# Kernel optimization log

Hardware: AMD Instinct MI355X
Metric: run time of the kernel (lower is better)

Reference implementation:

```python
import jax, jax.numpy as jnp
import numpy as np

N_NODES = 100000
N_EDGES = 1600000
D_IN = 128
D_HID = 128
D_OUT = 128


def setup_inputs() -> dict:
    key = jax.random.key(0)
    ks = jax.random.split(key, 12)
    x = jax.random.normal(ks[0], (N_NODES, D_IN), dtype=jnp.float32)
    edge_index = jax.random.randint(ks[1], (2, N_EDGES), 0, N_NODES, dtype=jnp.int64)
    s = 0.05
    # GraphConv layer l: out = agg @ w_rel + x @ w_root + b  (lin_rel has bias, lin_root does not)
    w_rel1 = jax.random.normal(ks[2], (D_IN, D_HID), dtype=jnp.float32) * s
    w_root1 = jax.random.normal(ks[3], (D_IN, D_HID), dtype=jnp.float32) * s
    b1 = jax.random.normal(ks[4], (D_HID,), dtype=jnp.float32) * s
    w_rel2 = jax.random.normal(ks[5], (D_HID, D_HID), dtype=jnp.float32) * s
    w_root2 = jax.random.normal(ks[6], (D_HID, D_HID), dtype=jnp.float32) * s
    b2 = jax.random.normal(ks[7], (D_HID,), dtype=jnp.float32) * s
    w_rel3 = jax.random.normal(ks[8], (D_HID, D_OUT), dtype=jnp.float32) * s
    w_root3 = jax.random.normal(ks[9], (D_HID, D_OUT), dtype=jnp.float32) * s
    b3 = jax.random.normal(ks[10], (D_OUT,), dtype=jnp.float32) * s
    return {"x": x, "edge_index": edge_index,
            "w_rel1": w_rel1, "w_root1": w_root1, "b1": b1,
            "w_rel2": w_rel2, "w_root2": w_root2, "b2": b2,
            "w_rel3": w_rel3, "w_root3": w_root3, "b3": b3}


def _graph_conv(h, src, dst, w_rel, w_root, b):
    # sum-aggregate neighbor features (message = x_j, flow src -> dst),
    # then linear; identical math to PyG GraphConv with aggr='add'.
    agg = jax.ops.segment_sum(h[src], dst, num_segments=h.shape[0])
    return agg @ w_rel + h @ w_root + b


def reference(x, edge_index, w_rel1, w_root1, b1, w_rel2, w_root2, b2, w_rel3, w_root3, b3):
    src, dst = edge_index[0], edge_index[1]
    h = jax.nn.relu(_graph_conv(x, src, dst, w_rel1, w_root1, b1))
    h = jax.nn.relu(_graph_conv(h, src, dst, w_rel2, w_root2, b2))
    out = _graph_conv(h, src, dst, w_rel3, w_root3, b3)
    return out
```

## Files before the change

kernel.cpp:

```cpp
#include <hip/hip_runtime.h>
#include <hip/hip_bf16.h>
#include <stdint.h>

typedef __hip_bfloat16 bf16;
typedef __hip_bfloat162 bf162;

typedef __attribute__((ext_vector_type(8))) short short8;
typedef __attribute__((ext_vector_type(4))) float floatx4;

#define BSH   8
#define BSZ   256
#define CHUNK 8192
#define NBMAX 512


__device__ __forceinline__ void acc2(float& a, float& b, unsigned u) {
    a += __uint_as_float(u << 16);
    b += __uint_as_float(u & 0xffff0000u);
}

__global__ __launch_bounds__(256)
void prep_kernel(const float* __restrict__ x, bf16* __restrict__ y, int n4, int nCvt,
                 const float* __restrict__ wr1, const float* __restrict__ wo1,
                 const float* __restrict__ wr2, const float* __restrict__ wo2,
                 const float* __restrict__ wr3, const float* __restrict__ wo3,
                 bf16* __restrict__ w1, bf16* __restrict__ w2, bf16* __restrict__ w3) {
    const int b = blockIdx.x;
    if (b < nCvt) {
        const int i = b * 256 + threadIdx.x;
        if (i < n4) {
            float4 v = ((const float4*)x)[i];
            bf162 a, c;
            a.x = __float2bfloat16(v.x); a.y = __float2bfloat16(v.y);
            c.x = __float2bfloat16(v.z); c.y = __float2bfloat16(v.w);
            ((bf162*)y)[i * 2]     = a;
            ((bf162*)y)[i * 2 + 1] = c;
        }
        return;
    }
    int t = (b - nCvt) * 256 + threadIdx.x;
    const int layer = t >> 12;
    t &= 4095;
    const float* wrel  = (layer == 0) ? wr1 : (layer == 1) ? wr2 : wr3;
    const float* wroot = (layer == 0) ? wo1 : (layer == 1) ? wo2 : wo3;
    bf16*        wsw   = (layer == 0) ? w1  : (layer == 1) ? w2  : w3;
    const int lane = t & 63;
    const int ct   = (t >> 6) & 7;
    const int kt   = t >> 9;
    const int kbase = kt * 32 + (lane >> 4) * 8;
    const int n     = ct * 16 + (lane & 15);
    bf16* q = wsw + (size_t)t * 8;
#pragma unroll
    for (int j = 0; j < 8; ++j) {
        const int k = kbase + j;
        const float v = (k < 128) ? wrel[k * 128 + n] : wroot[(k - 128) * 128 + n];
        q[j] = __float2bfloat16(v);
    }
}


__global__ __launch_bounds__(256)
void bhist_kernel(const int* __restrict__ dst, int* __restrict__ T,
                  int E, int NB, int GB) {
    __shared__ int lh[NBMAX];
    const int b = blockIdx.x;
    for (int u = threadIdx.x; u < NB; u += 256) lh[u] = 0;
    __syncthreads();
    const int beg = b * CHUNK, end = min(beg + CHUNK, E);
    for (int e = beg + threadIdx.x; e < end; e += 256)
        atomicAdd(&lh[dst[e] >> BSH], 1);
    __syncthreads();
    for (int u = threadIdx.x; u < NB; u += 256)
        T[u * GB + b] = lh[u];
}

__global__ __launch_bounds__(256)
void scan1_kernel(const int* __restrict__ deg, int* __restrict__ rp,
                  int* __restrict__ bsum, int n) {
    __shared__ int s[256];
    const int tid = threadIdx.x;
    const int i = blockIdx.x * 256 + tid;
    const int d = (i < n) ? deg[i] : 0;
    s[tid] = d;
    __syncthreads();
    for (int off = 1; off < 256; off <<= 1) {
        int u = (tid >= off) ? s[tid - off] : 0;
        __syncthreads();
        s[tid] += u;
        __syncthreads();
    }
    if (i < n) rp[i] = s[tid] - d;
    if (tid == 255) bsum[blockIdx.x] = s[255];
}

__global__ __launch_bounds__(512)
void scan2_kernel(int* __restrict__ bsum, int G) {
    __shared__ int s[512];
    const int tid = threadIdx.x;
    const int d = (tid < G) ? bsum[tid] : 0;
    s[tid] = d;
    __syncthreads();
    for (int off = 1; off < 512; off <<= 1) {
        int u = (tid >= off) ? s[tid - off] : 0;
        __syncthreads();
        s[tid] += u;
        __syncthreads();
    }
    if (tid < G) bsum[tid] = s[tid] - d;
}

__global__ __launch_bounds__(256)
void scan3_kernel(int* __restrict__ rp, const int* __restrict__ bsum, int n) {
    const int i = blockIdx.x * 256 + threadIdx.x;
    if (i < n) rp[i] += bsum[blockIdx.x];
}

__global__ __launch_bounds__(256)
void bscatter_kernel(const int* __restrict__ src, const int* __restrict__ dst,
                     const int* __restrict__ T, int* __restrict__ ebuf,
                     int E, int NB, int GB) {
    __shared__ int lofs[NBMAX];
    const int b = blockIdx.x;
    for (int u = threadIdx.x; u < NB; u += 256)
        lofs[u] = T[u * GB + b];
    __syncthreads();
    const int beg = b * CHUNK, end = min(beg + CHUNK, E);
    for (int e = beg + threadIdx.x; e < end; e += 256) {
        const int d = dst[e];
        const int u = d >> BSH;
        const int pos = atomicAdd(&lofs[u], 1);
        ebuf[pos] = (src[e] << BSH) | (d & (BSZ - 1));
    }
}

__global__ __launch_bounds__(256)
void bbuild_kernel(const int* __restrict__ T, const int* __restrict__ ebuf,
                   int* __restrict__ rp, int* __restrict__ col,
                   int E, int N, int NB, int GB) {
    __shared__ int s[256];
    __shared__ int lrank[256];
    const int u = blockIdx.x;
    const int tid = threadIdx.x;
    const int beg = T[u * GB];
    const int end = (u + 1 < NB) ? T[(u + 1) * GB] : E;

    lrank[tid] = 0;
    __syncthreads();
    for (int e = beg + tid; e < end; e += 256)
        atomicAdd(&lrank[ebuf[e] & (BSZ - 1)], 1);
    __syncthreads();
    const int cntv = lrank[tid];
    s[tid] = cntv;
    __syncthreads();
    for (int off = 1; off < 256; off <<= 1) {
        int v = (tid >= off) ? s[tid - off] : 0;
        __syncthreads();
        s[tid] += v;
        __syncthreads();
    }
    const int excl = s[tid] - cntv;
    const int node = u * BSZ + tid;
    if (node < N) rp[node] = beg + excl;
    if (u == NB - 1 && tid == 0) rp[N] = E;
    lrank[tid] = beg + excl;
    __syncthreads();
    for (int e = beg + tid; e < end; e += 256) {
        const int p = ebuf[e];
        const int pos = atomicAdd(&lrank[p & (BSZ - 1)], 1);
        col[pos] = p >> BSH;
    }
}


__global__ __launch_bounds__(512)
void agg_kernel(const bf16* __restrict__ h, const int* __restrict__ rp,
                const int* __restrict__ col, bf16* __restrict__ agg, int N) {
    const int lane = threadIdx.x & 63;
    const int wid  = threadIdx.x >> 6;
    const int node = blockIdx.x * 8 + wid;
    if (node >= N) return;
    const int half = lane >> 5;
    const int l32  = lane & 31;
    const int f    = l32 * 4;
    const int beg = rp[node], end = rp[node + 1];

    float acc[4] = {0.f, 0.f, 0.f, 0.f};
    int e = beg;
#pragma unroll 2
    for (; e + 8 <= end; e += 8) {
        const int s0 = col[e + half];
        const int s1 = col[e + 2 + half];
        const int s2 = col[e + 4 + half];
        const int s3 = col[e + 6 + half];
        const uint2 r0 = *(const uint2*)(h + (size_t)s0 * 128 + f);
        const uint2 r1 = *(const uint2*)(h + (size_t)s1 * 128 + f);
        const uint2 r2 = *(const uint2*)(h + (size_t)s2 * 128 + f);
        const uint2 r3 = *(const uint2*)(h + (size_t)s3 * 128 + f);
        acc2(acc[0], acc[1], r0.x); acc2(acc[2], acc[3], r0.y);
        acc2(acc[0], acc[1], r1.x); acc2(acc[2], acc[3], r1.y);
        acc2(acc[0], acc[1], r2.x); acc2(acc[2], acc[3], r2.y);
        acc2(acc[0], acc[1], r3.x); acc2(acc[2], acc[3], r3.y);
    }
    for (; e < end; e += 2) {
        const bool act = (e + half) < end;
        const int s = col[act ? (e + half) : e];
        const uint2 r = *(const uint2*)(h + (size_t)s * 128 + f);
        if (act) { acc2(acc[0], acc[1], r.x); acc2(acc[2], acc[3], r.y); }
    }

#pragma unroll
    for (int j = 0; j < 4; ++j)
        acc[j] += __shfl_xor(acc[j], 32, 64);

    if (half == 0) {
        bf162 o0, o1;
        o0.x = __float2bfloat16(acc[0]); o0.y = __float2bfloat16(acc[1]);
        o1.x = __float2bfloat16(acc[2]); o1.y = __float2bfloat16(acc[3]);
        bf162* q = (bf162*)(agg + (size_t)node * 128 + f);
        q[0] = o0;
        q[1] = o1;
    }
}


template <bool RELU, typename OT>
__global__ __launch_bounds__(256)
void mfma_gemm_kernel(const bf16* __restrict__ Aagg, const bf16* __restrict__ Hroot,
                      const bf16* __restrict__ wsw, const float* __restrict__ bias,
                      OT* __restrict__ out, int M) {
    const int tid  = threadIdx.x;
    const int lane = tid & 63;
    const int wave = tid >> 6;
    const int l15  = lane & 15;
    const int quad = lane >> 4;

    const int row_a = blockIdx.x * 64 + wave * 16 + l15;
    const bool rowok = row_a < M;

    floatx4 acc[8];
#pragma unroll
    for (int ct = 0; ct < 8; ++ct) acc[ct] = (floatx4){0.f, 0.f, 0.f, 0.f};

#pragma unroll
    for (int kt = 0; kt < 8; ++kt) {
        const bf16* Abase = (kt < 4) ? Aagg : Hroot;
        const int k0 = (kt & 3) * 32 + quad * 8;
        short8 afrag = (short8){0, 0, 0, 0, 0, 0, 0, 0};
        if (rowok) afrag = *(const short8*)(Abase + (size_t)row_a * 128 + k0);
#pragma unroll
        for (int ct = 0; ct < 8; ++ct) {
            const short8 bfrag = *(const short8*)(wsw + (size_t)((kt * 8 + ct) * 64 + lane) * 8);
            acc[ct] = __builtin_amdgcn_mfma_f32_16x16x32_bf16(afrag, bfrag, acc[ct], 0, 0, 0);
        }
    }

    const int row_o = blockIdx.x * 64 + wave * 16 + quad * 4;
#pragma unroll
    for (int ct = 0; ct < 8; ++ct) {
        const int colc = ct * 16 + l15;
        const float bv = bias[colc];
#pragma unroll
        for (int r = 0; r < 4; ++r) {
            const int row = row_o + r;
            if (row < M) {
                float v = acc[ct][r] + bv;
                if (RELU) v = fmaxf(v, 0.f);
                if constexpr (sizeof(OT) == 2)
                    ((bf16*)out)[(size_t)row * 128 + colc] = __float2bfloat16(v);
                else
                    ((float*)out)[(size_t)row * 128 + colc] = v;
            }
        }
    }
}


extern "C" void kernel_launch(void* const* d_in, const int* in_sizes, int n_in,
                              void* d_out, int out_size, void* d_ws, size_t ws_size,
                              hipStream_t stream) {
    const float* x       = (const float*)d_in[0];
    const int*   ei      = (const int*)d_in[1];
    const float* w_rel1  = (const float*)d_in[2];
    const float* w_root1 = (const float*)d_in[3];
    const float* b1      = (const float*)d_in[4];
    const float* w_rel2  = (const float*)d_in[5];
    const float* w_root2 = (const float*)d_in[6];
    const float* b2      = (const float*)d_in[7];
    const float* w_rel3  = (const float*)d_in[8];
    const float* w_root3 = (const float*)d_in[9];
    const float* b3      = (const float*)d_in[10];
    float* out = (float*)d_out;

    const int N = in_sizes[0] / 128;
    const int E = in_sizes[1] / 2;
    const int* src = ei;
    const int* dst = ei + E;

    char* w = (char*)d_ws;
    auto alloc = [&](size_t bytes) {
        char* p = w;
        w += (bytes + 255) & ~(size_t)255;
        return p;
    };
    int*  col  = (int*)alloc((size_t)E * 4);
    int*  rp   = (int*)alloc((size_t)(N + 1) * 4);
    bf16* h1   = (bf16*)alloc((size_t)N * 128 * 2);
    bf16* xbf  = (bf16*)alloc((size_t)N * 128 * 2);
    bf16* agg  = (bf16*)alloc((size_t)N * 128 * 2);
    bf16* wsw1 = (bf16*)alloc(32768 * 2);
    bf16* wsw2 = (bf16*)alloc(32768 * 2);
    bf16* wsw3 = (bf16*)alloc(32768 * 2);
    bf16* h2   = xbf;
    int*  T    = (int*)h1;
    int*  bsum = (int*)(h1 + 1024 * 1024);
    int*  ebuf = (int*)agg;

    const int NB = (N + BSZ - 1) / BSZ;
    const int GB = (E + CHUNK - 1) / CHUNK;
    const int nT = NB * GB;
    const int scanTBlocks = (nT + 255) / 256;

    const int aggBlocks  = (N + 7) / 8;
    const int gemmBlocks = (N + 63) / 64;
    const int cvtBlocks  = (N * 32 + 255) / 256;

    prep_kernel<<<cvtBlocks + 48, 256, 0, stream>>>(
        x, xbf, N * 32, cvtBlocks,
        w_rel1, w_root1, w_rel2, w_root2, w_rel3, w_root3,
        wsw1, wsw2, wsw3);

    bhist_kernel<<<GB, 256, 0, stream>>>(dst, T, E, NB, GB);
    scan1_kernel<<<scanTBlocks, 256, 0, stream>>>(T, T, bsum, nT);
    scan2_kernel<<<1, 512, 0, stream>>>(bsum, scanTBlocks);
    scan3_kernel<<<scanTBlocks, 256, 0, stream>>>(T, bsum, nT);
    bscatter_kernel<<<GB, 256, 0, stream>>>(src, dst, T, ebuf, E, NB, GB);
    bbuild_kernel<<<NB, 256, 0, stream>>>(T, ebuf, rp, col, E, N, NB, GB);

    agg_kernel<<<aggBlocks, 512, 0, stream>>>(xbf, rp, col, agg, N);
    mfma_gemm_kernel<true, bf16><<<gemmBlocks, 256, 0, stream>>>(agg, xbf, wsw1, b1, h1, N);
    agg_kernel<<<aggBlocks, 512, 0, stream>>>(h1, rp, col, agg, N);
    mfma_gemm_kernel<true, bf16><<<gemmBlocks, 256, 0, stream>>>(agg, h1, wsw2, b2, h2, N);
    agg_kernel<<<aggBlocks, 512, 0, stream>>>(h2, rp, col, agg, N);
    mfma_gemm_kernel<false, float><<<gemmBlocks, 256, 0, stream>>>(agg, h2, wsw3, b3, out, N);
}
```

Before: 475.8 us.

## Fuse whole GNN pipeline into one cooperative persistent kernel with grid syncs

Replaces the chain of prep, CSR build, aggregation and GEMM launches with a single cooperative kernel that uses grid.sync() between phases. The goal is to remove per-launch overhead and inter-kernel gaps. The CSR build also switches from the bucketed histogram/scatter scheme to plain global atomics on degree and cursor arrays. This risks heavy atomic contention, limits parallelism to the resident grid, and makes the per-node edge order within each CSR row nondeterministic. The old multi-kernel path is kept as a fallback if the cooperative launch fails.

```diff
diff --git a/kernel.cpp b/kernel.cpp
--- a/kernel.cpp
+++ b/kernel.cpp
@@ -1,4 +1,5 @@
 #include <hip/hip_runtime.h>
+#include <hip/hip_cooperative_groups.h>
 #include <hip/hip_bf16.h>
 #include <stdint.h>
 
@@ -18,6 +19,237 @@
     a += __uint_as_float(u << 16);
     b += __uint_as_float(u & 0xffff0000u);
 }
+
+
+struct MegaArgs {
+    const float* x;
+    const int*   ei;
+    const float *wr1, *wo1, *wr2, *wo2, *wr3, *wo3;
+    const float *b1, *b2, *b3;
+    float* out;
+    bf16 *xbf, *h1, *aggb;
+    bf16 *wsw1, *wsw2, *wsw3;
+    int  *col, *rp, *cur, *deg, *Pb;
+    int N, E;
+};
+
+__global__ __launch_bounds__(256)
+void mega_kernel(MegaArgs a) {
+    namespace cg = cooperative_groups;
+    cg::grid_group grid = cg::this_grid();
+
+    __shared__ int sscan[256];
+
+    const int tid  = threadIdx.x;
+    const int gtid = blockIdx.x * blockDim.x + tid;
+    const int gsz  = gridDim.x * blockDim.x;
+    const int N = a.N, E = a.E;
+    const int* src = a.ei;
+    const int* dst = a.ei + E;
+
+    {
+        for (int i = gtid; i < N; i += gsz) a.deg[i] = 0;
+        const int n4 = N * 32;
+        for (int i = gtid; i < n4; i += gsz) {
+            float4 v = ((const float4*)a.x)[i];
+            bf162 p, q;
+            p.x = __float2bfloat16(v.x); p.y = __float2bfloat16(v.y);
+            q.x = __float2bfloat16(v.z); q.y = __float2bfloat16(v.w);
+            ((bf162*)a.xbf)[i * 2]     = p;
+            ((bf162*)a.xbf)[i * 2 + 1] = q;
+        }
+        for (int t = gtid; t < 3 * 4096; t += gsz) {
+            const int layer = t >> 12;
+            const int u = t & 4095;
+            const float* wrel  = (layer == 0) ? a.wr1 : (layer == 1) ? a.wr2 : a.wr3;
+            const float* wroot = (layer == 0) ? a.wo1 : (layer == 1) ? a.wo2 : a.wo3;
+            bf16*        wsw   = (layer == 0) ? a.wsw1 : (layer == 1) ? a.wsw2 : a.wsw3;
+            const int lane = u & 63;
+            const int ct   = (u >> 6) & 7;
+            const int kt   = u >> 9;
+            const int kbase = kt * 32 + (lane >> 4) * 8;
+            const int n     = ct * 16 + (lane & 15);
+            bf16* q = wsw + (size_t)u * 8;
+#pragma unroll
+            for (int j = 0; j < 8; ++j) {
+                const int k = kbase + j;
+                const float v = (k < 128) ? wrel[k * 128 + n] : wroot[(k - 128) * 128 + n];
+                q[j] = __float2bfloat16(v);
+            }
+        }
+    }
+    grid.sync();
+
+    for (int e = gtid; e < E; e += gsz)
+        atomicAdd(&a.deg[dst[e]], 1);
+    grid.sync();
+
+    const int C = (N + gridDim.x - 1) / gridDim.x;
+    {
+        const int base = blockIdx.x * C;
+        int carry = 0;
+        for (int off = 0; off < C; off += 256) {
+            const int idx = base + off + tid;
+            const bool ok = (off + tid < C) && (idx < N);
+            const int v = ok ? a.deg[idx] : 0;
+            sscan[tid] = v;
+            __syncthreads();
+            for (int d = 1; d < 256; d <<= 1) {
+                int u = (tid >= d) ? sscan[tid - d] : 0;
+                __syncthreads();
+                sscan[tid] += u;
+                __syncthreads();
+            }
+            if (ok) a.rp[idx] = carry + sscan[tid] - v;
+            const int tot = sscan[255];
+            __syncthreads();
+            carry += tot;
+        }
+        if (tid == 0) a.Pb[blockIdx.x] = carry;
+    }
+    grid.sync();
+
+    if (blockIdx.x == 0) {
+        const int G = gridDim.x;
+        int carry = 0;
+        for (int off = 0; off < G; off += 256) {
+            const int i = off + tid;
+            const int v = (i < G) ? a.Pb[i] : 0;
+            sscan[tid] = v;
+            __syncthreads();
+            for (int d = 1; d < 256; d <<= 1) {
+                int u = (tid >= d) ? sscan[tid - d] : 0;
+                __syncthreads();
+                sscan[tid] += u;
+                __syncthreads();
+            }
+            if (i < G) a.Pb[i] = carry + sscan[tid] - v;
+            const int tot = sscan[255];
+            __syncthreads();
+            carry += tot;
+        }
+    }
+    grid.sync();
+
+    {
+        const int base = blockIdx.x * C;
+        const int o = a.Pb[blockIdx.x];
+        for (int off = tid; off < C; off += 256) {
+            const int idx = base + off;
+            if (idx < N) {
+                const int r = a.rp[idx] + o;
+                a.rp[idx]  = r;
+                a.cur[idx] = r;
+            }
+        }
+        if (gtid == 0) a.rp[N] = E;
+    }
+    grid.sync();
+
+    for (int e = gtid; e < E; e += gsz) {
+        const int d = dst[e];
+        const int p = atomicAdd(&a.cur[d], 1);
+        a.col[p] = src[e];
+    }
+    grid.sync();
+
+    const int lane = tid & 63;
+    const int wid  = tid >> 6;
+    const int nwaves = gsz >> 6;
+    const int half = lane >> 5;
+    const int l32  = lane & 31;
+    const int f    = l32 * 4;
+    const int l15  = lane & 15;
+    const int quad = lane >> 4;
+    const int tiles = (N + 63) >> 6;
+
+    for (int L = 0; L < 3; ++L) {
+        const bf16* Hin = (L == 0) ? a.xbf : (L == 1) ? a.h1 : a.xbf;
+        bf16*  houtb = (L == 0) ? a.h1 : a.xbf;
+        const bf16* wsw = (L == 0) ? a.wsw1 : (L == 1) ? a.wsw2 : a.wsw3;
+        const float* bias = (L == 0) ? a.b1 : (L == 1) ? a.b2 : a.b3;
+
+        for (int node = blockIdx.x * 4 + wid; node < N; node += nwaves) {
+            const int beg = a.rp[node], end = a.rp[node + 1];
+            float acc[4] = {0.f, 0.f, 0.f, 0.f};
+            int e = beg;
+#pragma unroll 2
+            for (; e + 8 <= end; e += 8) {
+                const int s0 = a.col[e + half];
+                const int s1 = a.col[e + 2 + half];
+                const int s2 = a.col[e + 4 + half];
+                const int s3 = a.col[e + 6 + half];
+                const uint2 r0 = *(const uint2*)(Hin + (size_t)s0 * 128 + f);
+                const uint2 r1 = *(const uint2*)(Hin + (size_t)s1 * 128 + f);
+                const uint2 r2 = *(const uint2*)(Hin + (size_t)s2 * 128 + f);
+                const uint2 r3 = *(const uint2*)(Hin + (size_t)s3 * 128 + f);
+                acc2(acc[0], acc[1], r0.x); acc2(acc[2], acc[3], r0.y);
+                acc2(acc[0], acc[1], r1.x); acc2(acc[2], acc[3], r1.y);
+                acc2(acc[0], acc[1], r2.x); acc2(acc[2], acc[3], r2.y);
+                acc2(acc[0], acc[1], r3.x); acc2(acc[2], acc[3], r3.y);
+            }
+            for (; e < end; e += 2) {
+                const bool act = (e + half) < end;
+                const int s = a.col[act ? (e + half) : e];
+                const uint2 r = *(const uint2*)(Hin + (size_t)s * 128 + f);
+                if (act) { acc2(acc[0], acc[1], r.x); acc2(acc[2], acc[3], r.y); }
+            }
+#pragma unroll
+            for (int j = 0; j < 4; ++j)
+                acc[j] += __shfl_xor(acc[j], 32, 64);
+            if (half == 0) {
+                bf162 o0, o1;
+                o0.x = __float2bfloat16(acc[0]); o0.y = __float2bfloat16(acc[1]);
+                o1.x = __float2bfloat16(acc[2]); o1.y = __float2bfloat16(acc[3]);
+                bf162* q = (bf162*)(a.aggb + (size_t)node * 128 + f);
+                q[0] = o0;
+                q[1] = o1;
+            }
+        }
+        grid.sync();
+
+        for (int tb = blockIdx.x; tb < tiles; tb += gridDim.x) {
+            const int row_a = tb * 64 + wid * 16 + l15;
+            const bool rowok = row_a < N;
+            floatx4 acc[8];
+#pragma unroll
+            for (int ct = 0; ct < 8; ++ct) acc[ct] = (floatx4){0.f, 0.f, 0.f, 0.f};
+#pragma unroll
+            for (int kt = 0; kt < 8; ++kt) {
+                const bf16* Abase = (kt < 4) ? a.aggb : Hin;
+                const int k0 = (kt & 3) * 32 + quad * 8;
+                short8 afrag = (short8){0, 0, 0, 0, 0, 0, 0, 0};
+                if (rowok) afrag = *(const short8*)(Abase + (size_t)row_a * 128 + k0);
+#pragma unroll
+                for (int ct = 0; ct < 8; ++ct) {
+                    const short8 bfrag = *(const short8*)(wsw + (size_t)((kt * 8 + ct) * 64 + lane) * 8);
+                    acc[ct] = __builtin_amdgcn_mfma_f32_16x16x32_bf16(afrag, bfrag, acc[ct], 0, 0, 0);
+                }
+            }
+            const int row_o = tb * 64 + wid * 16 + quad * 4;
+#pragma unroll
+            for (int ct = 0; ct < 8; ++ct) {
+                const int colc = ct * 16 + l15;
+                const float bv = bias[colc];
+#pragma unroll
+                for (int r = 0; r < 4; ++r) {
+                    const int row = row_o + r;
+                    if (row < N) {
+                        float v = acc[ct][r] + bv;
+                        if (L < 2) {
+                            v = fmaxf(v, 0.f);
+                            houtb[(size_t)row * 128 + colc] = __float2bfloat16(v);
+                        } else {
+                            a.out[(size_t)row * 128 + colc] = v;
+                        }
+                    }
+                }
+            }
+        }
+        if (L < 2) grid.sync();
+    }
+}
+
 
 __global__ __launch_bounds__(256)
 void prep_kernel(const float* __restrict__ x, bf16* __restrict__ y, int n4, int nCvt,
@@ -58,7 +290,6 @@
     }
 }
 
-
 __global__ __launch_bounds__(256)
 void bhist_kernel(const int* __restrict__ dst, int* __restrict__ T,
                   int E, int NB, int GB) {
@@ -170,7 +401,6 @@
         col[pos] = p >> BSH;
     }
 }
-
 
 __global__ __launch_bounds__(512)
 void agg_kernel(const bf16* __restrict__ h, const int* __restrict__ rp,
@@ -207,11 +437,9 @@
         const uint2 r = *(const uint2*)(h + (size_t)s * 128 + f);
         if (act) { acc2(acc[0], acc[1], r.x); acc2(acc[2], acc[3], r.y); }
     }
-
 #pragma unroll
     for (int j = 0; j < 4; ++j)
         acc[j] += __shfl_xor(acc[j], 32, 64);
-
     if (half == 0) {
         bf162 o0, o1;
         o0.x = __float2bfloat16(acc[0]); o0.y = __float2bfloat16(acc[1]);
@@ -221,7 +449,6 @@
         q[1] = o1;
     }
 }
-
 
 template <bool RELU, typename OT>
 __global__ __launch_bounds__(256)
@@ -304,16 +531,49 @@
     };
     int*  col  = (int*)alloc((size_t)E * 4);
     int*  rp   = (int*)alloc((size_t)(N + 1) * 4);
+    int*  cur  = (int*)alloc((size_t)N * 4);
+    int*  deg  = (int*)alloc((size_t)N * 4);
+    int*  Pb   = (int*)alloc(4096 * 4);
     bf16* h1   = (bf16*)alloc((size_t)N * 128 * 2);
     bf16* xbf  = (bf16*)alloc((size_t)N * 128 * 2);
-    bf16* agg  = (bf16*)alloc((size_t)N * 128 * 2);
+    bf16* aggb = (bf16*)alloc((size_t)N * 128 * 2);
     bf16* wsw1 = (bf16*)alloc(32768 * 2);
     bf16* wsw2 = (bf16*)alloc(32768 * 2);
     bf16* wsw3 = (bf16*)alloc(32768 * 2);
-    bf16* h2   = xbf;
-    int*  T    = (int*)h1;
-    int*  bsum = (int*)(h1 + 1024 * 1024);
-    int*  ebuf = (int*)agg;
+
+    static int maxGrid = 0;
+    if (maxGrid == 0) {
+        int perCU = 0, nCU = 0, dev = 0;
+        hipError_t e1 = hipGetDevice(&dev);
+        hipError_t e2 = hipDeviceGetAttribute(&nCU, hipDeviceAttributeMultiprocessorCount, dev);
+        hipError_t e3 = hipOccupancyMaxActiveBlocksPerMultiprocessor(&perCU, mega_kernel, 256, 0);
+        if (e1 == hipSuccess && e2 == hipSuccess && e3 == hipSuccess && perCU > 0 && nCU > 0)
+            maxGrid = perCU * nCU;
+        else
+            maxGrid = -1;
+    }
+
+    if (maxGrid > 0) {
+        const int grid = (maxGrid < 2048) ? maxGrid : 2048;
+        MegaArgs ma;
+        ma.x = x; ma.ei = ei;
+        ma.wr1 = w_rel1; ma.wo1 = w_root1; ma.wr2 = w_rel2; ma.wo2 = w_root2;
+        ma.wr3 = w_rel3; ma.wo3 = w_root3;
+        ma.b1 = b1; ma.b2 = b2; ma.b3 = b3;
+        ma.out = out;
+        ma.xbf = xbf; ma.h1 = h1; ma.aggb = aggb;
+        ma.wsw1 = wsw1; ma.wsw2 = wsw2; ma.wsw3 = wsw3;
+        ma.col = col; ma.rp = rp; ma.cur = cur; ma.deg = deg; ma.Pb = Pb;
+        ma.N = N; ma.E = E;
+        void* args[] = {&ma};
+        if (hipLaunchCooperativeKernel((const void*)mega_kernel, dim3(grid), dim3(256),
+                                       args, 0, stream) == hipSuccess)
+            return;
+    }
+
+    int* T    = (int*)h1;
+    int* bsum = (int*)(h1 + 1024 * 1024);
+    int* ebuf = (int*)aggb;
 
     const int NB = (N + BSZ - 1) / BSZ;
     const int GB = (E + CHUNK - 1) / CHUNK;
@@ -336,10 +596,10 @@
     bscatter_kernel<<<GB, 256, 0, stream>>>(src, dst, T, ebuf, E, NB, GB);
     bbuild_kernel<<<NB, 256, 0, stream>>>(T, ebuf, rp, col, E, N, NB, GB);
 
-    agg_kernel<<<aggBlocks, 512, 0, stream>>>(xbf, rp, col, agg, N);
-    mfma_gemm_kernel<true, bf16><<<gemmBlocks, 256, 0, stream>>>(agg, xbf, wsw1, b1, h1, N);
-    agg_kernel<<<aggBlocks, 512, 0, stream>>>(h1, rp, col, agg, N);
-    mfma_gemm_kernel<true, bf16><<<gemmBlocks, 256, 0, stream>>>(agg, h1, wsw2, b2, h2, N);
-    agg_kernel<<<aggBlocks, 512, 0, stream>>>(h2, rp, col, agg, N);
-    mfma_gemm_kernel<false, float><<<gemmBlocks, 256, 0, stream>>>(agg, h2, wsw3, b3, out, N);
-}
+    agg_kernel<<<aggBlocks, 512, 0, stream>>>(xbf, rp, col, aggb, N);
+    mfma_gemm_kernel<true, bf16><<<gemmBlocks, 256, 0, stream>>>(aggb, xbf, wsw1, b1, h1, N);
+    agg_kernel<<<aggBlocks, 512, 0, stream>>>(h1, rp, col, aggb, N);
+    mfma_gemm_kernel<true, bf16><<<gemmBlocks, 256, 0, stream>>>(aggb, h1, wsw2, b2, xbf, N);
+    agg_kernel<<<aggBlocks, 512, 0, stream>>>(xbf, rp, col, aggb, N);
+    mfma_gemm_kernel<false, float><<<gemmBlocks, 256, 0, stream>>>(aggb, xbf, wsw3, b3, out, N);
+}
```

After: 1.461 ms. 3.07x slower.

## Stage GEMM weights and output tile in LDS, fuse histogram and scan fixup

Applied to the files above, without the earlier changes.

The GEMM kernel now loads the swizzled weight matrix into shared memory once per block, processes 128 rows per 512-thread block, and writes results through a shared-memory tile so global stores are coalesced 16-byte vectors. The edge histogram is merged into the input-conversion kernel, and the third scan pass is removed by adding block sums directly in the scatter and build kernels. These target repeated global weight reads, scattered 2-byte stores and launch overhead. The large shared-memory footprint may reduce occupancy.

```diff
diff --git a/kernel.cpp b/kernel.cpp
--- a/kernel.cpp
+++ b/kernel.cpp
@@ -20,11 +20,14 @@
 }
 
 __global__ __launch_bounds__(256)
-void prep_kernel(const float* __restrict__ x, bf16* __restrict__ y, int n4, int nCvt,
-                 const float* __restrict__ wr1, const float* __restrict__ wo1,
-                 const float* __restrict__ wr2, const float* __restrict__ wo2,
-                 const float* __restrict__ wr3, const float* __restrict__ wo3,
-                 bf16* __restrict__ w1, bf16* __restrict__ w2, bf16* __restrict__ w3) {
+void prep_bhist_kernel(const float* __restrict__ x, bf16* __restrict__ y, int n4, int nCvt,
+                       const float* __restrict__ wr1, const float* __restrict__ wo1,
+                       const float* __restrict__ wr2, const float* __restrict__ wo2,
+                       const float* __restrict__ wr3, const float* __restrict__ wo3,
+                       bf16* __restrict__ w1, bf16* __restrict__ w2, bf16* __restrict__ w3,
+                       const int* __restrict__ dst, int* __restrict__ T,
+                       int E, int NB, int GB) {
+    __shared__ int lh[NBMAX];
     const int b = blockIdx.x;
     if (b < nCvt) {
         const int i = b * 256 + threadIdx.x;
@@ -38,41 +41,38 @@
         }
         return;
     }
-    int t = (b - nCvt) * 256 + threadIdx.x;
-    const int layer = t >> 12;
-    t &= 4095;
-    const float* wrel  = (layer == 0) ? wr1 : (layer == 1) ? wr2 : wr3;
-    const float* wroot = (layer == 0) ? wo1 : (layer == 1) ? wo2 : wo3;
-    bf16*        wsw   = (layer == 0) ? w1  : (layer == 1) ? w2  : w3;
-    const int lane = t & 63;
-    const int ct   = (t >> 6) & 7;
-    const int kt   = t >> 9;
-    const int kbase = kt * 32 + (lane >> 4) * 8;
-    const int n     = ct * 16 + (lane & 15);
-    bf16* q = wsw + (size_t)t * 8;
-#pragma unroll
-    for (int j = 0; j < 8; ++j) {
-        const int k = kbase + j;
-        const float v = (k < 128) ? wrel[k * 128 + n] : wroot[(k - 128) * 128 + n];
-        q[j] = __float2bfloat16(v);
-    }
-}
-
-
-__global__ __launch_bounds__(256)
-void bhist_kernel(const int* __restrict__ dst, int* __restrict__ T,
-                  int E, int NB, int GB) {
-    __shared__ int lh[NBMAX];
-    const int b = blockIdx.x;
+    if (b < nCvt + 48) {
+        int t = (b - nCvt) * 256 + threadIdx.x;
+        const int layer = t >> 12;
+        t &= 4095;
+        const float* wrel  = (layer == 0) ? wr1 : (layer == 1) ? wr2 : wr3;
+        const float* wroot = (layer == 0) ? wo1 : (layer == 1) ? wo2 : wo3;
+        bf16*        wsw   = (layer == 0) ? w1  : (layer == 1) ? w2  : w3;
+        const int lane = t & 63;
+        const int ct   = (t >> 6) & 7;
+        const int kt   = t >> 9;
+        const int kbase = kt * 32 + (lane >> 4) * 8;
+        const int n     = ct * 16 + (lane & 15);
+        bf16* q = wsw + (size_t)t * 8;
+#pragma unroll
+        for (int j = 0; j < 8; ++j) {
+            const int k = kbase + j;
+            const float v = (k < 128) ? wrel[k * 128 + n] : wroot[(k - 128) * 128 + n];
+            q[j] = __float2bfloat16(v);
+        }
+        return;
+    }
+    const int bb = b - nCvt - 48;
     for (int u = threadIdx.x; u < NB; u += 256) lh[u] = 0;
     __syncthreads();
-    const int beg = b * CHUNK, end = min(beg + CHUNK, E);
+    const int beg = bb * CHUNK, end = min(beg + CHUNK, E);
     for (int e = beg + threadIdx.x; e < end; e += 256)
         atomicAdd(&lh[dst[e] >> BSH], 1);
     __syncthreads();
     for (int u = threadIdx.x; u < NB; u += 256)
-        T[u * GB + b] = lh[u];
-}
+        T[u * GB + bb] = lh[u];
+}
+
 
 __global__ __launch_bounds__(256)
 void scan1_kernel(const int* __restrict__ deg, int* __restrict__ rp,
@@ -109,20 +109,17 @@
     if (tid < G) bsum[tid] = s[tid] - d;
 }
 
-__global__ __launch_bounds__(256)
-void scan3_kernel(int* __restrict__ rp, const int* __restrict__ bsum, int n) {
-    const int i = blockIdx.x * 256 + threadIdx.x;
-    if (i < n) rp[i] += bsum[blockIdx.x];
-}
 
 __global__ __launch_bounds__(256)
 void bscatter_kernel(const int* __restrict__ src, const int* __restrict__ dst,
-                     const int* __restrict__ T, int* __restrict__ ebuf,
-                     int E, int NB, int GB) {
+                     const int* __restrict__ T, const int* __restrict__ bsum,
+                     int* __restrict__ ebuf, int E, int NB, int GB) {
     __shared__ int lofs[NBMAX];
     const int b = blockIdx.x;
-    for (int u = threadIdx.x; u < NB; u += 256)
-        lofs[u] = T[u * GB + b];
+    for (int u = threadIdx.x; u < NB; u += 256) {
+        const int idx = u * GB + b;
+        lofs[u] = T[idx] + bsum[idx >> 8];
+    }
     __syncthreads();
     const int beg = b * CHUNK, end = min(beg + CHUNK, E);
     for (int e = beg + threadIdx.x; e < end; e += 256) {
@@ -134,15 +131,18 @@
 }
 
 __global__ __launch_bounds__(256)
-void bbuild_kernel(const int* __restrict__ T, const int* __restrict__ ebuf,
+void bbuild_kernel(const int* __restrict__ T, const int* __restrict__ bsum,
+                   const int* __restrict__ ebuf,
                    int* __restrict__ rp, int* __restrict__ col,
                    int E, int N, int NB, int GB) {
     __shared__ int s[256];
     __shared__ int lrank[256];
     const int u = blockIdx.x;
     const int tid = threadIdx.x;
-    const int beg = T[u * GB];
-    const int end = (u + 1 < NB) ? T[(u + 1) * GB] : E;
+    const int i0 = u * GB;
+    const int beg = T[i0] + bsum[i0 >> 8];
+    const int i1 = (u + 1) * GB;
+    const int end = (u + 1 < NB) ? (T[i1] + bsum[i1 >> 8]) : E;
 
     lrank[tid] = 0;
     __syncthreads();
@@ -207,11 +207,9 @@
         const uint2 r = *(const uint2*)(h + (size_t)s * 128 + f);
         if (act) { acc2(acc[0], acc[1], r.x); acc2(acc[2], acc[3], r.y); }
     }
-
 #pragma unroll
     for (int j = 0; j < 4; ++j)
         acc[j] += __shfl_xor(acc[j], 32, 64);
-
     if (half == 0) {
         bf162 o0, o1;
         o0.x = __float2bfloat16(acc[0]); o0.y = __float2bfloat16(acc[1]);
@@ -224,18 +222,28 @@
 
 
 template <bool RELU, typename OT>
-__global__ __launch_bounds__(256)
+__global__ __launch_bounds__(512)
 void mfma_gemm_kernel(const bf16* __restrict__ Aagg, const bf16* __restrict__ Hroot,
                       const bf16* __restrict__ wsw, const float* __restrict__ bias,
                       OT* __restrict__ out, int M) {
-    const int tid  = threadIdx.x;
+    __shared__ __align__(16) char smem[67584];
+    const int tid = threadIdx.x;
+
+#pragma unroll
+    for (int i = 0; i < 8; ++i) {
+        const int off = i * 8192 + tid * 16;
+        *(float4*)(smem + off) = *(const float4*)((const char*)wsw + off);
+    }
+    __syncthreads();
+
     const int lane = tid & 63;
     const int wave = tid >> 6;
     const int l15  = lane & 15;
     const int quad = lane >> 4;
-
-    const int row_a = blockIdx.x * 64 + wave * 16 + l15;
+    const int base = blockIdx.x * 128;
+    const int row_a = base + wave * 16 + l15;
     const bool rowok = row_a < M;
+    const bf16* wl = (const bf16*)smem;
 
     floatx4 acc[8];
 #pragma unroll
@@ -249,27 +257,59 @@
         if (rowok) afrag = *(const short8*)(Abase + (size_t)row_a * 128 + k0);
 #pragma unroll
         for (int ct = 0; ct < 8; ++ct) {
-            const short8 bfrag = *(const short8*)(wsw + (size_t)((kt * 8 + ct) * 64 + lane) * 8);
+            const short8 bfrag = *(const short8*)(wl + (size_t)((kt * 8 + ct) * 64 + lane) * 8);
             acc[ct] = __builtin_amdgcn_mfma_f32_16x16x32_bf16(afrag, bfrag, acc[ct], 0, 0, 0);
         }
     }
 
-    const int row_o = blockIdx.x * 64 + wave * 16 + quad * 4;
-#pragma unroll
-    for (int ct = 0; ct < 8; ++ct) {
-        const int colc = ct * 16 + l15;
-        const float bv = bias[colc];
-#pragma unroll
-        for (int r = 0; r < 4; ++r) {
-            const int row = row_o + r;
-            if (row < M) {
+    __syncthreads();
+    const int rloc = wave * 16 + quad * 4;
+
+    if constexpr (sizeof(OT) == 2) {
+        bf16* tl = (bf16*)smem;
+#pragma unroll
+        for (int ct = 0; ct < 8; ++ct) {
+            const int colc = ct * 16 + l15;
+            const float bv = bias[colc];
+#pragma unroll
+            for (int r = 0; r < 4; ++r) {
                 float v = acc[ct][r] + bv;
                 if (RELU) v = fmaxf(v, 0.f);
-                if constexpr (sizeof(OT) == 2)
-                    ((bf16*)out)[(size_t)row * 128 + colc] = __float2bfloat16(v);
-                else
-                    ((float*)out)[(size_t)row * 128 + colc] = v;
+                tl[(rloc + r) * 136 + colc] = __float2bfloat16(v);
             }
+        }
+        __syncthreads();
+#pragma unroll
+        for (int i = 0; i < 4; ++i) {
+            const int chunk = i * 512 + tid;
+            const int row = chunk >> 4;
+            const int c   = chunk & 15;
+            if (base + row < M)
+                *(float4*)((char*)out + (size_t)(base + row) * 256 + c * 16) =
+                    *(const float4*)(smem + row * 272 + c * 16);
+        }
+    } else {
+        float* tl = (float*)smem;
+#pragma unroll
+        for (int ct = 0; ct < 8; ++ct) {
+            const int colc = ct * 16 + l15;
+            const float bv = bias[colc];
+#pragma unroll
+            for (int r = 0; r < 4; ++r) {
+                float v = acc[ct][r] + bv;
+                if (RELU) v = fmaxf(v, 0.f);
+                tl[(rloc + r) * 132 + colc] = v;
+            }
+        }
+        __syncthreads();
+#pragma unroll
+        for (int i = 0; i < 8; ++i) {
+            const int chunk = i * 512 + tid;
+            const int row = chunk >> 5;
+            const int c   = chunk & 31;
+            if (base + row < M)
+                *(float4*)((char*)out + (size_t)(base + row) * 512 + c * 16) =
+                    *(const float4*)(smem + row * 528 + c * 16);
         }
     }
 }
@@ -306,14 +346,14 @@
     int*  rp   = (int*)alloc((size_t)(N + 1) * 4);
     bf16* h1   = (bf16*)alloc((size_t)N * 128 * 2);
     bf16* xbf  = (bf16*)alloc((size_t)N * 128 * 2);
-    bf16* agg  = (bf16*)alloc((size_t)N * 128 * 2);
+    bf16* aggb = (bf16*)alloc((size_t)N * 128 * 2);
     bf16* wsw1 = (bf16*)alloc(32768 * 2);
     bf16* wsw2 = (bf16*)alloc(32768 * 2);
     bf16* wsw3 = (bf16*)alloc(32768 * 2);
     bf16* h2   = xbf;
     int*  T    = (int*)h1;
     int*  bsum = (int*)(h1 + 1024 * 1024);
-    int*  ebuf = (int*)agg;
+    int*  ebuf = (int*)aggb;
 
     const int NB = (N + BSZ - 1) / BSZ;
     const int GB = (E + CHUNK - 1) / CHUNK;
@@ -321,25 +361,24 @@
     const int scanTBlocks = (nT + 255) / 256;
 
     const int aggBlocks  = (N + 7) / 8;
-    const int gemmBlocks = (N + 63) / 64;
+    const int gemmBlocks = (N + 127) / 128;
     const int cvtBlocks  = (N * 32 + 255) / 256;
 
-    prep_kernel<<<cvtBlocks + 48, 256, 0, stream>>>(
+    prep_bhist_kernel<<<cvtBlocks + 48 + GB, 256, 0, stream>>>(
         x, xbf, N * 32, cvtBlocks,
         w_rel1, w_root1, w_rel2, w_root2, w_rel3, w_root3,
-        wsw1, wsw2, wsw3);
-
-    bhist_kernel<<<GB, 256, 0, stream>>>(dst, T, E, NB, GB);
+        wsw1, wsw2, wsw3,
+        dst, T, E, NB, GB);
+
     scan1_kernel<<<scanTBlocks, 256, 0, stream>>>(T, T, bsum, nT);
     scan2_kernel<<<1, 512, 0, stream>>>(bsum, scanTBlocks);
-    scan3_kernel<<<scanTBlocks, 256, 0, stream>>>(T, bsum, nT);
-    bscatter_kernel<<<GB, 256, 0, stream>>>(src, dst, T, ebuf, E, NB, GB);
-    bbuild_kernel<<<NB, 256, 0, stream>>>(T, ebuf, rp, col, E, N, NB, GB);
-
-    agg_kernel<<<aggBlocks, 512, 0, stream>>>(xbf, rp, col, agg, N);
-    mfma_gemm_kernel<true, bf16><<<gemmBlocks, 256, 0, stream>>>(agg, xbf, wsw1, b1, h1, N);
-    agg_kernel<<<aggBlocks, 512, 0, stream>>>(h1, rp, col, agg, N);
-    mfma_gemm_kernel<true, bf16><<<gemmBlocks, 256, 0, stream>>>(agg, h1, wsw2, b2, h2, N);
-    agg_kernel<<<aggBlocks, 512, 0, stream>>>(h2, rp, col, agg, N);
-    mfma_gemm_kernel<false, float><<<gemmBlocks, 256, 0, stream>>>(agg, h2, wsw3, b3, out, N);
-}
+    bscatter_kernel<<<GB, 256, 0, stream>>>(src, dst, T, bsum, ebuf, E, NB, GB);
+    bbuild_kernel<<<NB, 256, 0, stream>>>(T, bsum, ebuf, rp, col, E, N, NB, GB);
+
+    agg_kernel<<<aggBlocks, 512, 0, stream>>>(xbf, rp, col, aggb, N);
+    mfma_gemm_kernel<true, bf16><<<gemmBlocks, 512, 0, stream>>>(aggb, xbf, wsw1, b1, h1, N);
+    agg_kernel<<<aggBlocks, 512, 0, stream>>>(h1, rp, col, aggb, N);
+    mfma_gemm_kernel<true, bf16><<<gemmBlocks, 512, 0, stream>>>(aggb, h1, wsw2, b2, h2, N);
+    agg_kernel<<<aggBlocks, 512, 0, stream>>>(h2, rp, col, aggb, N);
+    mfma_gemm_kernel<false, float><<<gemmBlocks, 512, 0, stream>>>(aggb, h2, wsw3, b3, out, N);
+}
```

New measurement: 425.9 us (median of 2 runs). 1.12x faster.
